# Kernel optimization log

Hardware: AMD Instinct MI355X
Metric: run time of the kernel (lower is better)

The kernel has to match this reference:

```python
import jax, jax.numpy as jnp
import numpy as np

N, E, F_IN, HID, HEADS, G = 50000, 800000, 128, 128, 4, 512
NEG_SLOPE = 0.2


def setup_inputs() -> dict:
    key = jax.random.key(0)
    ks = jax.random.split(key, 16)
    x = jax.random.normal(ks[0], (N, F_IN), dtype=jnp.float32)
    edge_index = jax.random.randint(ks[1], (2, E), 0, N, dtype=jnp.int32)
    batch = jnp.sort(jax.random.randint(ks[2], (N,), 0, G, dtype=jnp.int32))
    s1 = 1.0 / np.sqrt(F_IN)
    s2 = 1.0 / np.sqrt(HEADS * HID)
    params = {
        "W1": jax.random.uniform(ks[3], (F_IN, HEADS * HID), jnp.float32, -s1, s1),
        "a_src1": jax.random.normal(ks[4], (HEADS, HID), jnp.float32) * s1,
        "a_dst1": jax.random.normal(ks[5], (HEADS, HID), jnp.float32) * s1,
        "b1": jnp.zeros((HEADS * HID,), jnp.float32),
        "W2": jax.random.uniform(ks[6], (HEADS * HID, HID), jnp.float32, -s2, s2),
        "a_src2": jax.random.normal(ks[7], (1, HID), jnp.float32) * s2,
        "a_dst2": jax.random.normal(ks[8], (1, HID), jnp.float32) * s2,
        "b2": jnp.zeros((HID,), jnp.float32),
        "Wl": jax.random.normal(ks[9], (HID, 1), jnp.float32) / np.sqrt(HID),
        "bl": jnp.zeros((1,), jnp.float32),
    }
    return dict(x=x, edge_index=edge_index, batch=batch, **params)


def _gat_conv(x, W, a_src, a_dst, b, src, dst, heads, out_ch):
    n = x.shape[0]
    h = (x @ W).reshape(n, heads, out_ch)                      # [N,H,C]
    asrc = jnp.sum(h * a_src, axis=-1)                          # [N,H]
    adst = jnp.sum(h * a_dst, axis=-1)                          # [N,H]
    logits = jax.nn.leaky_relu(asrc[src] + adst[dst], NEG_SLOPE)  # [E,H]
    m = jax.ops.segment_max(logits, dst, num_segments=n)        # stable softmax per dst
    e = jnp.exp(logits - m[dst])
    denom = jax.ops.segment_sum(e, dst, num_segments=n)
    alpha = e / denom[dst]                                      # [E,H]
    out = jax.ops.segment_sum(alpha[:, :, None] * h[src], dst, num_segments=n)
    return out.reshape(n, heads * out_ch) + b


def reference(x, edge_index, batch, W1, a_src1, a_dst1, b1, W2, a_src2, a_dst2, b2, Wl, bl):
    n = x.shape[0]
    loop = jnp.arange(n, dtype=edge_index.dtype)
    src = jnp.concatenate([edge_index[0], loop])  # add_self_loops=True (PyG default)
    dst = jnp.concatenate([edge_index[1], loop])
    h = _gat_conv(x, W1, a_src1, a_dst1, b1, src, dst, HEADS, HID)
    h = jax.nn.elu(h)
    h = _gat_conv(h, W2, a_src2, a_dst2, b2, src, dst, 1, HID)
    h = jax.nn.elu(h)
    # global_mean_pool
    sums = jax.ops.segment_sum(h, batch, num_segments=G)
    cnts = jax.ops.segment_sum(jnp.ones((n,), h.dtype), batch, num_segments=G)
    pooled = sums / jnp.maximum(cnts, 1.0)[:, None]
    return (pooled @ Wl + bl).squeeze()
```

## Files before the change

kernel.cpp:

```cpp
#include <hip/hip_runtime.h>
#include <math.h>

#define NEG_SLOPE 0.2f

typedef float f4 __attribute__((ext_vector_type(4)));
typedef __attribute__((ext_vector_type(8))) short short8;
typedef __attribute__((ext_vector_type(4))) float f32x4;
typedef unsigned short ushort_t;
typedef unsigned char uchar_t;

__device__ __forceinline__ float bf2f(unsigned short s) {
    unsigned u = ((unsigned)s) << 16;
    float f; __builtin_memcpy(&f, &u, 4); return f;
}
__device__ __forceinline__ unsigned short f2bf(float f) {
    unsigned u; __builtin_memcpy(&u, &f, 4);
    u = (u + 0x7FFFu + ((u >> 16) & 1u)) >> 16;
    return (unsigned short)u;
}
__device__ __forceinline__ void gload16(const void* g, void* l) {
    __builtin_amdgcn_global_load_lds((const __attribute__((address_space(1))) void*)g,
                                     (__attribute__((address_space(3))) void*)l, 16, 0, 0);
}

__global__ void hist_kernel(const int* __restrict__ ei, int E, int Et, int* __restrict__ deg) {
    int e = blockIdx.x * blockDim.x + threadIdx.x;
    if (e >= Et) return;
    int d = (e < E) ? ei[E + e] : (e - E);
    atomicAdd(&deg[d], 1);
}

__global__ __launch_bounds__(1024) void scan_local(const int* __restrict__ deg,
                                                   int* __restrict__ off,
                                                   int* __restrict__ btot, int n) {
    __shared__ int s_w[16];
    int tid = threadIdx.x, lane = tid & 63, wv = tid >> 6;
    int i = blockIdx.x * 1024 + tid;
    int v = (i < n) ? deg[i] : 0;
    int x = v;
    #pragma unroll
    for (int d = 1; d < 64; d <<= 1) {
        int y = __shfl_up(x, d);
        if (lane >= d) x += y;
    }
    if (lane == 63) s_w[wv] = x;
    __syncthreads();
    if (tid < 16) {
        int y = s_w[tid];
        int z = y;
        #pragma unroll
        for (int d = 1; d < 16; d <<= 1) {
            int t2 = __shfl_up(z, d);
            if (tid >= d) z += t2;
        }
        if (tid == 15) btot[blockIdx.x] = z;
        s_w[tid] = z - y;
    }
    __syncthreads();
    if (i < n) off[i] = s_w[wv] + (x - v);
}

__global__ void scan_base(int* __restrict__ btot, int nb) {
    int lane = threadIdx.x;
    int v = (lane < nb) ? btot[lane] : 0;
    int x = v;
    #pragma unroll
    for (int d = 1; d < 64; d <<= 1) {
        int y = __shfl_up(x, d);
        if (lane >= d) x += y;
    }
    int total = __shfl(x, nb - 1);
    if (lane < nb) btot[lane] = x - v;
    if (lane == 0) btot[nb] = total;
}

__global__ void scan_add(const int* __restrict__ btot, int* __restrict__ off,
                         int* __restrict__ cur, const int* __restrict__ batch,
                         int* __restrict__ gcnt, int n, int nb) {
    int i = blockIdx.x * blockDim.x + threadIdx.x;
    if (i < n) {
        int o = off[i] + btot[i >> 10];
        off[i] = o;
        cur[i] = o;
        atomicAdd(&gcnt[batch[i]], 1);
    } else if (i == n) {
        off[n] = btot[nb];
    }
}

__global__ void scatter_kernel(const int* __restrict__ ei, int E, int Et,
                               int* __restrict__ cur, int* __restrict__ csr) {
    int e = blockIdx.x * blockDim.x + threadIdx.x;
    if (e >= Et) return;
    int s, d;
    if (e < E) { s = ei[e]; d = ei[E + e]; }
    else       { s = d = e - E; }
    int p = atomicAdd(&cur[d], 1);
    csr[p] = s;
}

__global__ void cast_all(const float* __restrict__ x, const float* __restrict__ W1,
                         const float* __restrict__ W2, ushort_t* __restrict__ xb,
                         ushort_t* __restrict__ W1t, ushort_t* __restrict__ W2t,
                         int n_x, int pad_x) {
    int i = blockIdx.x * blockDim.x + threadIdx.x;
    if (i < pad_x) {
        xb[i] = f2bf(i < n_x ? x[i] : 0.f);
        return;
    }
    int k = i - pad_x;
    if (k < 128 * 512) {
        int r = k >> 9, c = k & 511;
        W1t[(size_t)c * 128 + r] = f2bf(W1[k]);
        return;
    }
    k -= 128 * 512;
    if (k < 512 * 128) {
        int r = k >> 7, c = k & 127;
        W2t[(size_t)c * 512 + r] = f2bf(W2[k]);
    }
}

template<int BN, int H>
__global__ __launch_bounds__(256) void gemm_q(const ushort_t* __restrict__ A,
                                              const ushort_t* __restrict__ Bt,
                                              uchar_t* __restrict__ Cq,
                                              float* __restrict__ Csc,
                                              const float* __restrict__ aw_src,
                                              const float* __restrict__ aw_dst,
                                              float* __restrict__ avs,
                                              float* __restrict__ avd,
                                              int K) {
    constexpr int CT = BN / 64;
    __shared__ __align__(16) ushort_t As[32 * 32];
    __shared__ __align__(16) ushort_t Bs[BN * 32];
    __shared__ float s_rm[4][32];
    __shared__ float s_rs[32];
    __shared__ float s_avp[2][4][32];
    const int t = threadIdx.x, w = t >> 6, lane = t & 63;
    const int r0 = blockIdx.x * 32;

    const ushort_t* Ag = A + (size_t)(r0 + w * 16 + (lane >> 2)) * K + (lane & 3) * 8;
    const ushort_t* Bg = Bt + (size_t)(w * (BN / 4) + (lane >> 2)) * K + (lane & 3) * 8;
    ushort_t* Al = As + w * 512;
    ushort_t* Bl = Bs + w * (BN / 4) * 32;

    f32x4 acc[2][CT] = {};
    for (int k0 = 0; k0 < K; k0 += 32) {
        __syncthreads();
        if (w < 2) gload16(Ag + k0, Al);
        #pragma unroll
        for (int m = 0; m < CT; m++)
            gload16(Bg + k0 + (size_t)m * 16 * K, Bl + m * 512);
        __syncthreads();
        short8 af[2], bf[CT];
        #pragma unroll
        for (int i = 0; i < 2; i++)
            af[i] = *(const short8*)(As + (i * 16 + (lane & 15)) * 32 + (lane >> 4) * 8);
        #pragma unroll
        for (int jj = 0; jj < CT; jj++)
            bf[jj] = *(const short8*)(Bs + (w * (BN / 4) + jj * 16 + (lane & 15)) * 32 + (lane >> 4) * 8);
        #pragma unroll
        for (int i = 0; i < 2; i++)
            #pragma unroll
            for (int jj = 0; jj < CT; jj++)
                acc[i][jj] = __builtin_amdgcn_mfma_f32_16x16x32_bf16(af[i], bf[jj], acc[i][jj], 0, 0, 0);
    }

    float mr[2][4];
    #pragma unroll
    for (int i = 0; i < 2; i++)
        #pragma unroll
        for (int r = 0; r < 4; r++) {
            float m = 0.f;
            #pragma unroll
            for (int jj = 0; jj < CT; jj++) m = fmaxf(m, fabsf(acc[i][jj][r]));
            mr[i][r] = m;
        }
    #pragma unroll
    for (int d = 1; d < 16; d <<= 1)
        #pragma unroll
        for (int i = 0; i < 2; i++)
            #pragma unroll
            for (int r = 0; r < 4; r++) mr[i][r] = fmaxf(mr[i][r], __shfl_xor(mr[i][r], d));
    if ((lane & 15) == 0) {
        #pragma unroll
        for (int i = 0; i < 2; i++)
            #pragma unroll
            for (int r = 0; r < 4; r++) s_rm[w][i * 16 + (lane >> 4) * 4 + r] = mr[i][r];
    }

    float asc[CT], adc[CT];
    #pragma unroll
    for (int jj = 0; jj < CT; jj++) {
        int c = w * (BN / 4) + jj * 16 + (lane & 15);
        asc[jj] = aw_src[c];
        adc[jj] = aw_dst[c];
    }
    #pragma unroll
    for (int i = 0; i < 2; i++) {
        #pragma unroll
        for (int r = 0; r < 4; r++) {
            float ps = 0.f, pd = 0.f;
            #pragma unroll
            for (int jj = 0; jj < CT; jj++) {
                float v = acc[i][jj][r];
                ps = fmaf(v, asc[jj], ps);
                pd = fmaf(v, adc[jj], pd);
            }
            #pragma unroll
            for (int d = 1; d < 16; d <<= 1) {
                ps += __shfl_xor(ps, d);
                pd += __shfl_xor(pd, d);
            }
            if ((lane & 15) == 0) {
                int row = i * 16 + (lane >> 4) * 4 + r;
                if constexpr (H == 4) {
                    avs[(size_t)(r0 + row) * 4 + w] = ps;
                    avd[(size_t)(r0 + row) * 4 + w] = pd;
                } else {
                    s_avp[0][w][row] = ps;
                    s_avp[1][w][row] = pd;
                }
            }
        }
    }
    __syncthreads();
    if (t < 32) {
        float rm = fmaxf(fmaxf(s_rm[0][t], s_rm[1][t]), fmaxf(s_rm[2][t], s_rm[3][t]));
        rm = fmaxf(rm, 1e-30f);
        Csc[r0 + t] = rm * (1.f / 127.f);
        s_rs[t] = 127.f / rm;
        if constexpr (H == 1) {
            avs[r0 + t] = s_avp[0][0][t] + s_avp[0][1][t] + s_avp[0][2][t] + s_avp[0][3][t];
            avd[r0 + t] = s_avp[1][0][t] + s_avp[1][1][t] + s_avp[1][2][t] + s_avp[1][3][t];
        }
    }
    __syncthreads();
    uchar_t* s_q = (uchar_t*)Bs;
    #pragma unroll
    for (int i = 0; i < 2; i++)
        #pragma unroll
        for (int jj = 0; jj < CT; jj++)
            #pragma unroll
            for (int r = 0; r < 4; r++) {
                int row = i * 16 + (lane >> 4) * 4 + r;
                int col = w * (BN / 4) + jj * 16 + (lane & 15);
                int qi = (int)rintf(acc[i][jj][r] * s_rs[row]) + 128;
                qi = min(255, max(0, qi));
                s_q[row * BN + col] = (uchar_t)qi;
            }
    __syncthreads();
    constexpr int PASSES = BN / 128;
    constexpr int CPR = BN / 16;
    #pragma unroll
    for (int p2 = 0; p2 < PASSES; p2++) {
        int idx = p2 * 256 + t;
        int row = idx / CPR, ch = idx % CPR;
        *(uint4*)(Cq + (size_t)(r0 + row) * BN + ch * 16) =
            *(const uint4*)(s_q + row * BN + ch * 16);
    }
}

template<int H, int TOT, bool OUT_BF16>
__global__ __launch_bounds__(256) void agg_q(const int* __restrict__ off,
                                             const int* __restrict__ csr,
                                             const uchar_t* __restrict__ fq,
                                             const float* __restrict__ fs,
                                             const float* __restrict__ avs,
                                             const float* __restrict__ avd,
                                             const float* __restrict__ bias,
                                             void* __restrict__ outv, int n) {
    constexpr int J = TOT / 64;
    __shared__ float s_ex[4][64 * H];
    int w = threadIdx.x >> 6, lane = threadIdx.x & 63;
    int dst = blockIdx.x * 4 + w;
    if (dst >= n) return;
    const int h_own = (H == 1) ? 0 : (lane >> 4);
    float adv[H];
    if constexpr (H == 4) {
        f4 t4 = *(const f4*)&avd[(size_t)dst * 4];
        #pragma unroll
        for (int h = 0; h < 4; h++) adv[h] = t4[h];
    } else {
        adv[0] = avd[dst];
    }
    int beg = off[dst], end = off[dst + 1];
    float den[H] = {}, Ssum[H] = {};
    float acc[J] = {};
    float* exw = s_ex[w];

    for (int b = beg; b < end; b += 64) {
        int idx = b + lane;
        bool val = idx < end;
        int sv = val ? csr[idx] : 0;
        float srow = fs[sv];
        unsigned myoff = (unsigned)sv * TOT;
        if constexpr (H == 4) {
            f4 av = *(const f4*)&avs[(size_t)sv * 4];
            f4 exv;
            #pragma unroll
            for (int h = 0; h < 4; h++) {
                float l = av[h] + adv[h];
                l = fmaxf(l, l * NEG_SLOPE);
                float e = val ? __expf(l) : 0.f;
                den[h] += e;
                float es = e * srow;
                Ssum[h] += es;
                exv[h] = es;
            }
            *(f4*)&exw[lane * 4] = exv;
        } else {
            float l = avs[sv] + adv[0];
            l = fmaxf(l, l * NEG_SLOPE);
            float e = val ? __expf(l) : 0.f;
            den[0] += e;
            float es = e * srow;
            Ssum[0] += es;
            exw[lane] = es;
        }
        asm volatile("s_waitcnt lgkmcnt(0)" ::: "memory");
        int cnt = min(64, end - b);
        int j = 0;
        for (; j + 2 <= cnt; j += 2) {
            float e0 = exw[j * H + h_own];
            float e1 = exw[(j + 1) * H + h_own];
            unsigned v0 = (unsigned)__shfl((int)myoff, j) + lane * J;
            unsigned v1 = (unsigned)__shfl((int)myoff, j + 1) + lane * J;
            if constexpr (J == 8) {
                uint2 u0 = *(const uint2*)(fq + v0);
                uint2 u1 = *(const uint2*)(fq + v1);
                acc[0] += e0 * (float)(u0.x & 0xffu);
                acc[1] += e0 * (float)((u0.x >> 8) & 0xffu);
                acc[2] += e0 * (float)((u0.x >> 16) & 0xffu);
                acc[3] += e0 * (float)(u0.x >> 24);
                acc[4] += e0 * (float)(u0.y & 0xffu);
                acc[5] += e0 * (float)((u0.y >> 8) & 0xffu);
                acc[6] += e0 * (float)((u0.y >> 16) & 0xffu);
                acc[7] += e0 * (float)(u0.y >> 24);
                acc[0] += e1 * (float)(u1.x & 0xffu);
                acc[1] += e1 * (float)((u1.x >> 8) & 0xffu);
                acc[2] += e1 * (float)((u1.x >> 16) & 0xffu);
                acc[3] += e1 * (float)(u1.x >> 24);
                acc[4] += e1 * (float)(u1.y & 0xffu);
                acc[5] += e1 * (float)((u1.y >> 8) & 0xffu);
                acc[6] += e1 * (float)((u1.y >> 16) & 0xffu);
                acc[7] += e1 * (float)(u1.y >> 24);
            } else {
                unsigned us0 = *(const ushort_t*)(fq + v0);
                unsigned us1 = *(const ushort_t*)(fq + v1);
                acc[0] += e0 * (float)(us0 & 0xffu);
                acc[1] += e0 * (float)(us0 >> 8);
                acc[0] += e1 * (float)(us1 & 0xffu);
                acc[1] += e1 * (float)(us1 >> 8);
            }
        }
        if (j < cnt) {
            float e0 = exw[j * H + h_own];
            unsigned v0 = (unsigned)__shfl((int)myoff, j) + lane * J;
            if constexpr (J == 8) {
                uint2 u0 = *(const uint2*)(fq + v0);
                acc[0] += e0 * (float)(u0.x & 0xffu);
                acc[1] += e0 * (float)((u0.x >> 8) & 0xffu);
                acc[2] += e0 * (float)((u0.x >> 16) & 0xffu);
                acc[3] += e0 * (float)(u0.x >> 24);
                acc[4] += e0 * (float)(u0.y & 0xffu);
                acc[5] += e0 * (float)((u0.y >> 8) & 0xffu);
                acc[6] += e0 * (float)((u0.y >> 16) & 0xffu);
                acc[7] += e0 * (float)(u0.y >> 24);
            } else {
                unsigned us0 = *(const ushort_t*)(fq + v0);
                acc[0] += e0 * (float)(us0 & 0xffu);
                acc[1] += e0 * (float)(us0 >> 8);
            }
        }
    }
    #pragma unroll
    for (int h = 0; h < H; h++) {
        #pragma unroll
        for (int d = 32; d; d >>= 1) {
            den[h] += __shfl_xor(den[h], d);
            Ssum[h] += __shfl_xor(Ssum[h], d);
        }
    }
    float dh, Sh;
    if constexpr (H == 4) {
        dh = (lane & 32) ? ((lane & 16) ? den[3] : den[2]) : ((lane & 16) ? den[1] : den[0]);
        Sh = (lane & 32) ? ((lane & 16) ? Ssum[3] : Ssum[2]) : ((lane & 16) ? Ssum[1] : Ssum[0]);
    } else {
        dh = den[0]; Sh = Ssum[0];
    }
    float rden = 1.f / dh;
    if constexpr (OUT_BF16) {
        unsigned short ov[J];
        #pragma unroll
        for (int u = 0; u < J; u++) {
            float v = (acc[u] - 128.f * Sh) * rden + bias[lane * J + u];
            v = v > 0.f ? v : expm1f(v);
            ov[u] = f2bf(v);
        }
        *(short8*)((ushort_t*)outv + (size_t)dst * TOT + lane * J) = *(short8*)ov;
    } else {
        float v0 = (acc[0] - 128.f * Sh) * rden + bias[lane * 2];
        float v1 = (acc[1] - 128.f * Sh) * rden + bias[lane * 2 + 1];
        v0 = v0 > 0.f ? v0 : expm1f(v0);
        v1 = v1 > 0.f ? v1 : expm1f(v1);
        float2 vv = make_float2(v0, v1);
        *(float2*)((float*)outv + (size_t)dst * TOT + lane * 2) = vv;
    }
}

__global__ __launch_bounds__(256) void pool_kernel(const float* __restrict__ feat,
                                                   const int* __restrict__ batch,
                                                   float* __restrict__ gsum, int n) {
    int t = threadIdx.x;
    int ch = t & 127, half = t >> 7;
    int base = blockIdx.x * 64;
    float acc = 0.f;
    int curg = -1;
    for (int k = half; k < 64; k += 2) {
        int node = base + k;
        if (node >= n) break;
        int g = batch[node];
        if (g != curg) {
            if (curg >= 0) atomicAdd(&gsum[(size_t)curg * 128 + ch], acc);
            acc = 0.f;
            curg = g;
        }
        acc += feat[(size_t)node * 128 + ch];
    }
    if (curg >= 0) atomicAdd(&gsum[(size_t)curg * 128 + ch], acc);
}

__global__ __launch_bounds__(256) void final_kernel(const float* __restrict__ gsum,
                                                    const int* __restrict__ gcnt,
                                                    const float* __restrict__ Wl,
                                                    const float* __restrict__ bl,
                                                    float* __restrict__ out, int g_total) {
    int w = threadIdx.x >> 6, lane = threadIdx.x & 63;
    int g = blockIdx.x * 4 + w;
    if (g >= g_total) return;
    float inv = 1.f / fmaxf((float)gcnt[g], 1.f);
    float p = 0.f;
    #pragma unroll
    for (int j = 0; j < 2; j++) {
        int ch = lane + 64 * j;
        p += gsum[(size_t)g * 128 + ch] * Wl[ch];
    }
    #pragma unroll
    for (int d = 32; d; d >>= 1) p += __shfl_xor(p, d);
    if (lane == 0) out[g] = p * inv + bl[0];
}

extern "C" void kernel_launch(void* const* d_in, const int* in_sizes, int n_in,
                              void* d_out, int out_size, void* d_ws, size_t ws_size,
                              hipStream_t stream) {
    const float* x   = (const float*)d_in[0];
    const int*   ei  = (const int*)d_in[1];
    const int*   bat = (const int*)d_in[2];
    const float* W1  = (const float*)d_in[3];
    const float* as1 = (const float*)d_in[4];
    const float* ad1 = (const float*)d_in[5];
    const float* b1  = (const float*)d_in[6];
    const float* W2  = (const float*)d_in[7];
    const float* as2 = (const float*)d_in[8];
    const float* ad2 = (const float*)d_in[9];
    const float* b2  = (const float*)d_in[10];
    const float* Wl  = (const float*)d_in[11];
    const float* bl  = (const float*)d_in[12];
    float* out = (float*)d_out;

    const int N    = in_sizes[0] / 128;
    const int E    = in_sizes[1] / 2;
    const int Et   = E + N;
    const int G    = 512;
    const int Mpad = (N + 127) & ~127;
    const int nb   = (N + 1023) >> 10;

    char* p = (char*)d_ws;
    auto alloc = [&](size_t bytes) { char* r = p; p += (bytes + 255) & ~(size_t)255; return r; };
    ushort_t* xb    = (ushort_t*)alloc((size_t)Mpad * 128 * 2);
    ushort_t* W1t   = (ushort_t*)alloc((size_t)512 * 128 * 2);
    ushort_t* W2t   = (ushort_t*)alloc((size_t)128 * 512 * 2);
    uchar_t*  h1q   = (uchar_t*)alloc((size_t)Mpad * 512);
    float*    h1s   = (float*)alloc((size_t)Mpad * 4);
    ushort_t* hb    = (ushort_t*)alloc((size_t)Mpad * 512 * 2);
    uchar_t*  h2q   = (uchar_t*)alloc((size_t)Mpad * 128);
    float*    h2s   = (float*)alloc((size_t)Mpad * 4);
    float*    feat2 = (float*)alloc((size_t)N * 128 * 4);
    float*    avs1  = (float*)alloc((size_t)Mpad * 4 * 4);
    float*    avd1  = (float*)alloc((size_t)Mpad * 4 * 4);
    float*    avs2  = (float*)alloc((size_t)Mpad * 4);
    float*    avd2  = (float*)alloc((size_t)Mpad * 4);
    float*    gsum  = (float*)alloc((size_t)G * 128 * 4);
    int*      gcnt  = (int*)alloc((size_t)G * 4);
    int*      deg   = (int*)alloc((size_t)N * 4);
    int*      off   = (int*)alloc((size_t)(N + 1) * 4);
    int*      cur   = (int*)alloc((size_t)N * 4);
    int*      btot  = (int*)alloc((size_t)128 * 4);
    int*      csr   = (int*)alloc((size_t)Et * 4);

    hipMemsetAsync(gsum, 0, (size_t)((char*)off - (char*)gsum), stream);
    hipMemsetAsync(hb + (size_t)N * 512, 0, (size_t)(Mpad - N) * 512 * 2, stream);

    hist_kernel<<<(Et + 255) / 256, 256, 0, stream>>>(ei, E, Et, deg);
    scan_local<<<nb, 1024, 0, stream>>>(deg, off, btot, N);
    scan_base<<<1, 64, 0, stream>>>(btot, nb);
    scan_add<<<(N + 256) / 256, 256, 0, stream>>>(btot, off, cur, bat, gcnt, N, nb);
    cast_all<<<((Mpad * 128 + 2 * 65536) + 255) / 256, 256, 0, stream>>>(x, W1, W2, xb, W1t, W2t,
                                                                         N * 128, Mpad * 128);
    scatter_kernel<<<(Et + 255) / 256, 256, 0, stream>>>(ei, E, Et, cur, csr);

    gemm_q<512, 4><<<Mpad / 32, 256, 0, stream>>>(xb, W1t, h1q, h1s, as1, ad1, avs1, avd1, 128);
    agg_q<4, 512, true><<<(N + 3) / 4, 256, 0, stream>>>(off, csr, h1q, h1s, avs1, avd1, b1, hb, N);

    gemm_q<128, 1><<<Mpad / 32, 256, 0, stream>>>(hb, W2t, h2q, h2s, as2, ad2, avs2, avd2, 512);
    agg_q<1, 128, false><<<(N + 3) / 4, 256, 0, stream>>>(off, csr, h2q, h2s, avs2, avd2, b2, feat2, N);

    pool_kernel<<<(N + 63) / 64, 256, 0, stream>>>(feat2, bat, gsum, N);
    final_kernel<<<(G + 3) / 4, 256, 0, stream>>>(gsum, gcnt, Wl, bl, out, G);
}
```

Baseline: 441.7 us.

## Retile quantizing GEMM to 128x128 tiles with per-head scales and packed side data

Replaces the 32-row GEMM, which loaded the full column width per block, with a 128x128 tiled MFMA GEMM. Each block covers one head's columns, so the int8 scale becomes per row and per head. The source attention logit and the scale are packed into one interleaved side array, so the aggregation kernel fetches both in a single vector load. Byte-to-float unpacking in the aggregation loop now uses v_cvt_f32_ubyte instructions with fmaf. The intent is better operand reuse in the GEMM and fewer instructions and loads per edge in aggregation. The trade-offs are a slightly different quantization granularity and fewer, larger blocks for the second GEMM.

```diff
diff --git a/kernel.cpp b/kernel.cpp
--- a/kernel.cpp
+++ b/kernel.cpp
@@ -21,6 +21,12 @@
 __device__ __forceinline__ void gload16(const void* g, void* l) {
     __builtin_amdgcn_global_load_lds((const __attribute__((address_space(1))) void*)g,
                                      (__attribute__((address_space(3))) void*)l, 16, 0, 0);
+}
+__device__ __forceinline__ void cvt4(unsigned u, float& a, float& b, float& c, float& d) {
+    asm("v_cvt_f32_ubyte0 %0, %1" : "=v"(a) : "v"(u));
+    asm("v_cvt_f32_ubyte1 %0, %1" : "=v"(b) : "v"(u));
+    asm("v_cvt_f32_ubyte2 %0, %1" : "=v"(c) : "v"(u));
+    asm("v_cvt_f32_ubyte3 %0, %1" : "=v"(d) : "v"(u));
 }
 
 __global__ void hist_kernel(const int* __restrict__ ei, int E, int Et, int* __restrict__ deg) {
@@ -121,144 +127,113 @@
     }
 }
 
-template<int BN, int H>
-__global__ __launch_bounds__(256) void gemm_q(const ushort_t* __restrict__ A,
-                                              const ushort_t* __restrict__ Bt,
-                                              uchar_t* __restrict__ Cq,
-                                              float* __restrict__ Csc,
-                                              const float* __restrict__ aw_src,
-                                              const float* __restrict__ aw_dst,
-                                              float* __restrict__ avs,
-                                              float* __restrict__ avd,
-                                              int K) {
-    constexpr int CT = BN / 64;
-    __shared__ __align__(16) ushort_t As[32 * 32];
-    __shared__ __align__(16) ushort_t Bs[BN * 32];
-    __shared__ float s_rm[4][32];
-    __shared__ float s_rs[32];
-    __shared__ float s_avp[2][4][32];
+template<int H>
+__global__ __launch_bounds__(256) void gemm_q128(const ushort_t* __restrict__ A,
+                                                 const ushort_t* __restrict__ Bt,
+                                                 uchar_t* __restrict__ Cq,
+                                                 const float* __restrict__ aw_src,
+                                                 const float* __restrict__ aw_dst,
+                                                 float* __restrict__ side,
+                                                 float* __restrict__ avd,
+                                                 int K) {
+    const int Nc = H * 128;
+    __shared__ __align__(16) ushort_t As[128 * 32];
+    __shared__ __align__(16) ushort_t Bs[128 * 32];
+    __shared__ float s_red[3][2][128];
+    __shared__ float s_rs[128];
+    __shared__ __align__(16) uchar_t s_q[128 * 144];
     const int t = threadIdx.x, w = t >> 6, lane = t & 63;
-    const int r0 = blockIdx.x * 32;
-
-    const ushort_t* Ag = A + (size_t)(r0 + w * 16 + (lane >> 2)) * K + (lane & 3) * 8;
-    const ushort_t* Bg = Bt + (size_t)(w * (BN / 4) + (lane >> 2)) * K + (lane & 3) * 8;
-    ushort_t* Al = As + w * 512;
-    ushort_t* Bl = Bs + w * (BN / 4) * 32;
-
-    f32x4 acc[2][CT] = {};
+    const int r0 = blockIdx.x * 128, hb = blockIdx.y, c0 = hb * 128;
+    const int wr = w & 1, wc = w >> 1;
+
+    const ushort_t* Ag = A + (size_t)(r0 + w * 32 + (lane >> 2)) * K + (lane & 3) * 8;
+    const ushort_t* Bg = Bt + (size_t)(c0 + w * 32 + (lane >> 2)) * K + (lane & 3) * 8;
+    ushort_t* Al = As + w * 1024;
+    ushort_t* Bl = Bs + w * 1024;
+
+    f32x4 acc[4][4] = {};
     for (int k0 = 0; k0 < K; k0 += 32) {
         __syncthreads();
-        if (w < 2) gload16(Ag + k0, Al);
-        #pragma unroll
-        for (int m = 0; m < CT; m++)
-            gload16(Bg + k0 + (size_t)m * 16 * K, Bl + m * 512);
+        gload16(Ag + k0, Al);
+        gload16(Ag + k0 + (size_t)16 * K, Al + 512);
+        gload16(Bg + k0, Bl);
+        gload16(Bg + k0 + (size_t)16 * K, Bl + 512);
         __syncthreads();
-        short8 af[2], bf[CT];
-        #pragma unroll
-        for (int i = 0; i < 2; i++)
-            af[i] = *(const short8*)(As + (i * 16 + (lane & 15)) * 32 + (lane >> 4) * 8);
-        #pragma unroll
-        for (int jj = 0; jj < CT; jj++)
-            bf[jj] = *(const short8*)(Bs + (w * (BN / 4) + jj * 16 + (lane & 15)) * 32 + (lane >> 4) * 8);
-        #pragma unroll
-        for (int i = 0; i < 2; i++)
+        short8 af[4], bf[4];
+        #pragma unroll
+        for (int i = 0; i < 4; i++) {
+            af[i] = *(const short8*)(As + (wr * 64 + i * 16 + (lane & 15)) * 32 + (lane >> 4) * 8);
+            bf[i] = *(const short8*)(Bs + (wc * 64 + i * 16 + (lane & 15)) * 32 + (lane >> 4) * 8);
+        }
+        #pragma unroll
+        for (int i = 0; i < 4; i++)
             #pragma unroll
-            for (int jj = 0; jj < CT; jj++)
+            for (int jj = 0; jj < 4; jj++)
                 acc[i][jj] = __builtin_amdgcn_mfma_f32_16x16x32_bf16(af[i], bf[jj], acc[i][jj], 0, 0, 0);
     }
 
-    float mr[2][4];
-    #pragma unroll
-    for (int i = 0; i < 2; i++)
-        #pragma unroll
-        for (int r = 0; r < 4; r++) {
-            float m = 0.f;
-            #pragma unroll
-            for (int jj = 0; jj < CT; jj++) m = fmaxf(m, fabsf(acc[i][jj][r]));
-            mr[i][r] = m;
-        }
-    #pragma unroll
-    for (int d = 1; d < 16; d <<= 1)
-        #pragma unroll
-        for (int i = 0; i < 2; i++)
-            #pragma unroll
-            for (int r = 0; r < 4; r++) mr[i][r] = fmaxf(mr[i][r], __shfl_xor(mr[i][r], d));
-    if ((lane & 15) == 0) {
-        #pragma unroll
-        for (int i = 0; i < 2; i++)
-            #pragma unroll
-            for (int r = 0; r < 4; r++) s_rm[w][i * 16 + (lane >> 4) * 4 + r] = mr[i][r];
-    }
-
-    float asc[CT], adc[CT];
-    #pragma unroll
-    for (int jj = 0; jj < CT; jj++) {
-        int c = w * (BN / 4) + jj * 16 + (lane & 15);
+    float asc[4], adc[4];
+    #pragma unroll
+    for (int jj = 0; jj < 4; jj++) {
+        int c = c0 + wc * 64 + jj * 16 + (lane & 15);
         asc[jj] = aw_src[c];
         adc[jj] = aw_dst[c];
     }
     #pragma unroll
-    for (int i = 0; i < 2; i++) {
+    for (int i = 0; i < 4; i++) {
         #pragma unroll
         for (int r = 0; r < 4; r++) {
-            float ps = 0.f, pd = 0.f;
+            float m = 0.f, ps = 0.f, pd = 0.f;
             #pragma unroll
-            for (int jj = 0; jj < CT; jj++) {
+            for (int jj = 0; jj < 4; jj++) {
                 float v = acc[i][jj][r];
+                m = fmaxf(m, fabsf(v));
                 ps = fmaf(v, asc[jj], ps);
                 pd = fmaf(v, adc[jj], pd);
             }
             #pragma unroll
             for (int d = 1; d < 16; d <<= 1) {
+                m = fmaxf(m, __shfl_xor(m, d));
                 ps += __shfl_xor(ps, d);
                 pd += __shfl_xor(pd, d);
             }
             if ((lane & 15) == 0) {
-                int row = i * 16 + (lane >> 4) * 4 + r;
-                if constexpr (H == 4) {
-                    avs[(size_t)(r0 + row) * 4 + w] = ps;
-                    avd[(size_t)(r0 + row) * 4 + w] = pd;
-                } else {
-                    s_avp[0][w][row] = ps;
-                    s_avp[1][w][row] = pd;
-                }
+                int row = wr * 64 + i * 16 + (lane >> 4) * 4 + r;
+                s_red[0][wc][row] = m;
+                s_red[1][wc][row] = ps;
+                s_red[2][wc][row] = pd;
             }
         }
     }
     __syncthreads();
-    if (t < 32) {
-        float rm = fmaxf(fmaxf(s_rm[0][t], s_rm[1][t]), fmaxf(s_rm[2][t], s_rm[3][t]));
-        rm = fmaxf(rm, 1e-30f);
-        Csc[r0 + t] = rm * (1.f / 127.f);
+    if (t < 128) {
+        float rm = fmaxf(fmaxf(s_red[0][0][t], s_red[0][1][t]), 1e-30f);
         s_rs[t] = 127.f / rm;
-        if constexpr (H == 1) {
-            avs[r0 + t] = s_avp[0][0][t] + s_avp[0][1][t] + s_avp[0][2][t] + s_avp[0][3][t];
-            avd[r0 + t] = s_avp[1][0][t] + s_avp[1][1][t] + s_avp[1][2][t] + s_avp[1][3][t];
-        }
+        int node = r0 + t;
+        side[(size_t)node * (2 * H) + hb]     = s_red[1][0][t] + s_red[1][1][t];
+        side[(size_t)node * (2 * H) + H + hb] = rm * (1.f / 127.f);
+        avd[(size_t)node * H + hb]            = s_red[2][0][t] + s_red[2][1][t];
     }
     __syncthreads();
-    uchar_t* s_q = (uchar_t*)Bs;
-    #pragma unroll
-    for (int i = 0; i < 2; i++)
-        #pragma unroll
-        for (int jj = 0; jj < CT; jj++)
+    #pragma unroll
+    for (int i = 0; i < 4; i++)
+        #pragma unroll
+        for (int jj = 0; jj < 4; jj++)
             #pragma unroll
             for (int r = 0; r < 4; r++) {
-                int row = i * 16 + (lane >> 4) * 4 + r;
-                int col = w * (BN / 4) + jj * 16 + (lane & 15);
+                int row = wr * 64 + i * 16 + (lane >> 4) * 4 + r;
+                int col = wc * 64 + jj * 16 + (lane & 15);
                 int qi = (int)rintf(acc[i][jj][r] * s_rs[row]) + 128;
                 qi = min(255, max(0, qi));
-                s_q[row * BN + col] = (uchar_t)qi;
+                s_q[row * 144 + col] = (uchar_t)qi;
             }
     __syncthreads();
-    constexpr int PASSES = BN / 128;
-    constexpr int CPR = BN / 16;
-    #pragma unroll
-    for (int p2 = 0; p2 < PASSES; p2++) {
+    #pragma unroll
+    for (int p2 = 0; p2 < 4; p2++) {
         int idx = p2 * 256 + t;
-        int row = idx / CPR, ch = idx % CPR;
-        *(uint4*)(Cq + (size_t)(r0 + row) * BN + ch * 16) =
-            *(const uint4*)(s_q + row * BN + ch * 16);
+        int row = idx >> 3, ch = idx & 7;
+        *(uint4*)(Cq + (size_t)(r0 + row) * Nc + c0 + ch * 16) =
+            *(const uint4*)(s_q + row * 144 + ch * 16);
     }
 }
 
@@ -266,8 +241,7 @@
 __global__ __launch_bounds__(256) void agg_q(const int* __restrict__ off,
                                              const int* __restrict__ csr,
                                              const uchar_t* __restrict__ fq,
-                                             const float* __restrict__ fs,
-                                             const float* __restrict__ avs,
+                                             const float* __restrict__ side,
                                              const float* __restrict__ avd,
                                              const float* __restrict__ bias,
                                              void* __restrict__ outv, int n) {
@@ -290,14 +264,28 @@
     float acc[J] = {};
     float* exw = s_ex[w];
 
+    auto acc8 = [&](float e, uint2 u) {
+        float b0, b1, b2, b3;
+        cvt4(u.x, b0, b1, b2, b3);
+        acc[0] = fmaf(e, b0, acc[0]);
+        acc[1] = fmaf(e, b1, acc[1]);
+        acc[2] = fmaf(e, b2, acc[2]);
+        acc[3] = fmaf(e, b3, acc[3]);
+        cvt4(u.y, b0, b1, b2, b3);
+        acc[4] = fmaf(e, b0, acc[4]);
+        acc[5] = fmaf(e, b1, acc[5]);
+        acc[6] = fmaf(e, b2, acc[6]);
+        acc[7] = fmaf(e, b3, acc[7]);
+    };
+
     for (int b = beg; b < end; b += 64) {
         int idx = b + lane;
         bool val = idx < end;
         int sv = val ? csr[idx] : 0;
-        float srow = fs[sv];
         unsigned myoff = (unsigned)sv * TOT;
         if constexpr (H == 4) {
-            f4 av = *(const f4*)&avs[(size_t)sv * 4];
+            const f4* sp = (const f4*)(side + (size_t)sv * 8);
+            f4 av = sp[0], sc = sp[1];
             f4 exv;
             #pragma unroll
             for (int h = 0; h < 4; h++) {
@@ -305,17 +293,18 @@
                 l = fmaxf(l, l * NEG_SLOPE);
                 float e = val ? __expf(l) : 0.f;
                 den[h] += e;
-                float es = e * srow;
+                float es = e * sc[h];
                 Ssum[h] += es;
                 exv[h] = es;
             }
             *(f4*)&exw[lane * 4] = exv;
         } else {
-            float l = avs[sv] + adv[0];
+            float2 sp = *(const float2*)(side + (size_t)sv * 2);
+            float l = sp.x + adv[0];
             l = fmaxf(l, l * NEG_SLOPE);
             float e = val ? __expf(l) : 0.f;
             den[0] += e;
-            float es = e * srow;
+            float es = e * sp.y;
             Ssum[0] += es;
             exw[lane] = es;
         }
@@ -330,29 +319,20 @@
             if constexpr (J == 8) {
                 uint2 u0 = *(const uint2*)(fq + v0);
                 uint2 u1 = *(const uint2*)(fq + v1);
-                acc[0] += e0 * (float)(u0.x & 0xffu);
-                acc[1] += e0 * (float)((u0.x >> 8) & 0xffu);
-                acc[2] += e0 * (float)((u0.x >> 16) & 0xffu);
-                acc[3] += e0 * (float)(u0.x >> 24);
-                acc[4] += e0 * (float)(u0.y & 0xffu);
-                acc[5] += e0 * (float)((u0.y >> 8) & 0xffu);
-                acc[6] += e0 * (float)((u0.y >> 16) & 0xffu);
-                acc[7] += e0 * (float)(u0.y >> 24);
-                acc[0] += e1 * (float)(u1.x & 0xffu);
-                acc[1] += e1 * (float)((u1.x >> 8) & 0xffu);
-                acc[2] += e1 * (float)((u1.x >> 16) & 0xffu);
-                acc[3] += e1 * (float)(u1.x >> 24);
-                acc[4] += e1 * (float)(u1.y & 0xffu);
-                acc[5] += e1 * (float)((u1.y >> 8) & 0xffu);
-                acc[6] += e1 * (float)((u1.y >> 16) & 0xffu);
-                acc[7] += e1 * (float)(u1.y >> 24);
+                acc8(e0, u0);
+                acc8(e1, u1);
             } else {
                 unsigned us0 = *(const ushort_t*)(fq + v0);
                 unsigned us1 = *(const ushort_t*)(fq + v1);
-                acc[0] += e0 * (float)(us0 & 0xffu);
-                acc[1] += e0 * (float)(us0 >> 8);
-                acc[0] += e1 * (float)(us1 & 0xffu);
-                acc[1] += e1 * (float)(us1 >> 8);
+                float b0, b1;
+                asm("v_cvt_f32_ubyte0 %0, %1" : "=v"(b0) : "v"(us0));
+                asm("v_cvt_f32_ubyte1 %0, %1" : "=v"(b1) : "v"(us0));
+                acc[0] = fmaf(e0, b0, acc[0]);
+                acc[1] = fmaf(e0, b1, acc[1]);
+                asm("v_cvt_f32_ubyte0 %0, %1" : "=v"(b0) : "v"(us1));
+                asm("v_cvt_f32_ubyte1 %0, %1" : "=v"(b1) : "v"(us1));
+                acc[0] = fmaf(e1, b0, acc[0]);
+                acc[1] = fmaf(e1, b1, acc[1]);
             }
         }
         if (j < cnt) {
@@ -360,18 +340,14 @@
             unsigned v0 = (unsigned)__shfl((int)myoff, j) + lane * J;
             if constexpr (J == 8) {
                 uint2 u0 = *(const uint2*)(fq + v0);
-                acc[0] += e0 * (float)(u0.x & 0xffu);
-                acc[1] += e0 * (float)((u0.x >> 8) & 0xffu);
-                acc[2] += e0 * (float)((u0.x >> 16) & 0xffu);
-                acc[3] += e0 * (float)(u0.x >> 24);
-                acc[4] += e0 * (float)(u0.y & 0xffu);
-                acc[5] += e0 * (float)((u0.y >> 8) & 0xffu);
-                acc[6] += e0 * (float)((u0.y >> 16) & 0xffu);
-                acc[7] += e0 * (float)(u0.y >> 24);
+                acc8(e0, u0);
             } else {
                 unsigned us0 = *(const ushort_t*)(fq + v0);
-                acc[0] += e0 * (float)(us0 & 0xffu);
-                acc[1] += e0 * (float)(us0 >> 8);
+                float b0, b1;
+                asm("v_cvt_f32_ubyte0 %0, %1" : "=v"(b0) : "v"(us0));
+                asm("v_cvt_f32_ubyte1 %0, %1" : "=v"(b1) : "v"(us0));
+                acc[0] = fmaf(e0, b0, acc[0]);
+                acc[1] = fmaf(e0, b1, acc[1]);
             }
         }
     }
@@ -483,14 +459,12 @@
     ushort_t* W1t   = (ushort_t*)alloc((size_t)512 * 128 * 2);
     ushort_t* W2t   = (ushort_t*)alloc((size_t)128 * 512 * 2);
     uchar_t*  h1q   = (uchar_t*)alloc((size_t)Mpad * 512);
-    float*    h1s   = (float*)alloc((size_t)Mpad * 4);
     ushort_t* hb    = (ushort_t*)alloc((size_t)Mpad * 512 * 2);
     uchar_t*  h2q   = (uchar_t*)alloc((size_t)Mpad * 128);
-    float*    h2s   = (float*)alloc((size_t)Mpad * 4);
     float*    feat2 = (float*)alloc((size_t)N * 128 * 4);
-    float*    avs1  = (float*)alloc((size_t)Mpad * 4 * 4);
+    float*    side1 = (float*)alloc((size_t)Mpad * 8 * 4);
     float*    avd1  = (float*)alloc((size_t)Mpad * 4 * 4);
-    float*    avs2  = (float*)alloc((size_t)Mpad * 4);
+    float*    side2 = (float*)alloc((size_t)Mpad * 2 * 4);
     float*    avd2  = (float*)alloc((size_t)Mpad * 4);
     float*    gsum  = (float*)alloc((size_t)G * 128 * 4);
     int*      gcnt  = (int*)alloc((size_t)G * 4);
@@ -511,11 +485,11 @@
                                                                          N * 128, Mpad * 128);
     scatter_kernel<<<(Et + 255) / 256, 256, 0, stream>>>(ei, E, Et, cur, csr);
 
-    gemm_q<512, 4><<<Mpad / 32, 256, 0, stream>>>(xb, W1t, h1q, h1s, as1, ad1, avs1, avd1, 128);
-    agg_q<4, 512, true><<<(N + 3) / 4, 256, 0, stream>>>(off, csr, h1q, h1s, avs1, avd1, b1, hb, N);
-
-    gemm_q<128, 1><<<Mpad / 32, 256, 0, stream>>>(hb, W2t, h2q, h2s, as2, ad2, avs2, avd2, 512);
-    agg_q<1, 128, false><<<(N + 3) / 4, 256, 0, stream>>>(off, csr, h2q, h2s, avs2, avd2, b2, feat2, N);
+    gemm_q128<4><<<dim3(Mpad / 128, 4), 256, 0, stream>>>(xb, W1t, h1q, as1, ad1, side1, avd1, 128);
+    agg_q<4, 512, true><<<(N + 3) / 4, 256, 0, stream>>>(off, csr, h1q, side1, avd1, b1, hb, N);
+
+    gemm_q128<1><<<dim3(Mpad / 128, 1), 256, 0, stream>>>(hb, W2t, h2q, as2, ad2, side2, avd2, 512);
+    agg_q<1, 128, false><<<(N + 3) / 4, 256, 0, stream>>>(off, csr, h2q, side2, avd2, b2, feat2, N);
 
     pool_kernel<<<(N + 63) / 64, 256, 0, stream>>>(feat2, bat, gsum, N);
     final_kernel<<<(G + 3) / 4, 256, 0, stream>>>(gsum, gcnt, Wl, bl, out, G);
```

New measurement: 446.9 us. About the same (+1.2%).
